# Kernel tuning notes

Measured on AMD Instinct MI355X. Metric: run time of the kernel, lower is better.

The kernel has to match this reference:

```python
import jax, jax.numpy as jnp
import numpy as np

B, C, H, W = 8, 256, 80, 160   # 1/8-resolution feature maps of a 640x1280 stereo pair
DISP = 192 // 8                 # cost volume depth at 1/8 res
FACTOR = 2 ** 3                 # convex-upsample factor (n_downsample=3)
TOP_K = 3


def setup_inputs() -> dict:
    key = jax.random.key(0)
    k1, k2, k3 = jax.random.split(key, 3)
    return {
        "left": jax.random.normal(k1, (B, C, H, W), dtype=jnp.float32),
        "right": jax.random.normal(k2, (B, C, H, W), dtype=jnp.float32),
        "mask": jax.random.normal(k3, (B, 9 * FACTOR * FACTOR, H, W), dtype=jnp.float32),
        "iters": 12,
    }


def build_cost_volume(left, right):
    # cost[b,i,h,w] = mean_c left[b,c,h,w] * right[b,c,h,w-i], zero where w < i
    slices = []
    for i in range(DISP):  # fixed small structural loop over disparity shifts
        prod = jnp.mean(left[:, :, :, i:] * right[:, :, :, : W - i if i > 0 else W], axis=1)
        prod = jnp.pad(prod, ((0, 0), (0, 0), (i, 0)))
        slices.append(prod)
    return jnp.stack(slices, axis=1)  # [B, DISP, H, W]


def regression_topk(cost, k=TOP_K):
    # top-k over the disparity axis, softmax-weighted expectation of indices
    c = jnp.moveaxis(cost, 1, -1)            # [B, H, W, DISP]
    vals, inds = jax.lax.top_k(c, k)          # descending, like torch sort(1, True)[:, :k]
    w = jax.nn.softmax(vals, axis=-1)
    disp = jnp.sum(w * inds.astype(vals.dtype), axis=-1)
    return disp[:, None]                      # [B, 1, H, W]


def convex_upsample(flow, mask, iters):
    # Upsample [H,W] flow -> [8H,8W] via softmax convex combination of 3x3 neighbors.
    N, D, Hh, Ww = flow.shape
    temp = 1.0 + jnp.exp(-(jnp.float32(iters) - 1.0))  # training-mode temperature
    m = mask.reshape(N, 1, 9, FACTOR, FACTOR, Hh, Ww)
    m = jax.nn.softmax(m / temp, axis=2)
    fp = jnp.pad(FACTOR * flow, ((0, 0), (0, 0), (1, 1), (1, 1)))
    # 3x3 unfold in torch F.unfold row-major order: (dy, dx)
    patches = jnp.stack(
        [fp[:, :, dy:dy + Hh, dx:dx + Ww] for dy in range(3) for dx in range(3)], axis=2
    )  # [N, D, 9, H, W]
    up = jnp.sum(m * patches[:, :, :, None, None], axis=2)   # [N, D, F, F, H, W]
    up = up.transpose(0, 1, 4, 2, 5, 3)                      # [N, D, H, F, W, F]
    return up.reshape(N, D, FACTOR * Hh, FACTOR * Ww)


def reference(left, right, mask, iters):
    cost = build_cost_volume(left, right)
    init_disp = regression_topk(cost)                               # [B,1,H,W]
    # flow field (x-disparity channel + frozen y channel, as delta_flow[:,1]=0)
    flow = jnp.concatenate([init_disp, jnp.zeros_like(init_disp)], axis=1)
    flow_up = convex_upsample(flow, mask, iters)                    # [B,2,8H,8W]
    return -flow_up[:, :1]                                          # disparity prediction
```

## Files before the change

### kernel.cpp

```cpp
#include <hip/hip_runtime.h>
#include <cmath>

#define NBATCH 8
#define NCH    256
#define NH     80
#define NW     160
#define NDISP  24
#define FAC    8

constexpr int TPB1  = 128;
constexpr int WPB   = 2;
constexpr int NTILE = 5;
constexpr int SLOTS = 192;
constexpr int NBUF  = 2;
constexpr int NSTEP = 16;

typedef __attribute__((address_space(1))) unsigned int gu32;
typedef __attribute__((address_space(3))) unsigned int lu32;

#define LDS_AUX 2

__device__ __forceinline__ void gload_lds16(const float* g, float4* l) {
  __builtin_amdgcn_global_load_lds((gu32*)g, (lu32*)l, 16, 0, LDS_AUX);
}

template <int N>
__device__ __forceinline__ void wait_vm() {
  if constexpr (N == 3)      asm volatile("s_waitcnt vmcnt(3)" ::: "memory");
  else                       asm volatile("s_waitcnt vmcnt(0)" ::: "memory");
  __builtin_amdgcn_sched_barrier(0);
}

__device__ __forceinline__ void wait_lgkm0() {
  asm volatile("s_waitcnt lgkmcnt(0)" ::: "memory");
  __builtin_amdgcn_sched_barrier(0);
}

__device__ __forceinline__ float f4c(const float4& v, int k) {
  switch (k) { case 0: return v.x; case 1: return v.y; case 2: return v.z; default: return v.w; }
}

__global__ __launch_bounds__(TPB1) void cost_topk_kernel(
    const float* __restrict__ left, const float* __restrict__ right,
    float* __restrict__ disp)
{
  __shared__ float4 lds4[WPB][NBUF][SLOTS];

  const int lane = threadIdx.x & 63;
  const int widx = threadIdx.x >> 6;
  const int tileid = blockIdx.x;
  const int tile = tileid % NTILE;
  const int row  = tileid / NTILE;
  const int b    = row / NH;
  const int h    = row % NH;
  const int wb   = tile * 32;
  const int chb  = widx * NSTEP;

  const int cg = lane & 7;
  const int wq = lane >> 3;

  const size_t hw = (size_t)NH * NW;
  const float* lrow = left  + (size_t)b * NCH * hw + (size_t)h * NW;
  const float* rrow = right + (size_t)b * NCH * hw + (size_t)h * NW;

  const int c0 = lane >> 4,        q0 = (lane & 15) ^ c0;
  const int c1 = 4 + (lane >> 4),  q1 = (lane & 15) ^ c1;
  const int cl = lane >> 3,        wqs = (lane & 7) ^ cl;

  int off0 = wb - 32 + 4 * q0; if (off0 < 0) off0 = 0;
  int off1 = wb - 32 + 4 * q1; if (off1 < 0) off1 = 0;

  const float* srcR0 = rrow + (size_t)(c0 * 32 + chb) * hw + off0;
  const float* srcR1 = rrow + (size_t)(c1 * 32 + chb) * hw + off1;
  const float* srcL  = lrow + (size_t)(cl * 32 + chb) * hw + wb + 4 * wqs;

  float4* const wbase = &lds4[widx][0][0];

#define STAGE(BP) do {                               \
    gload_lds16(srcR0, (BP));                        \
    gload_lds16(srcR1, (BP) + 64);                   \
    gload_lds16(srcL,  (BP) + 128);                  \
    srcR0 += hw; srcR1 += hw; srcL += hw; } while (0)

  int rsl[7];
#pragma unroll
  for (int k = 0; k < 7; ++k) rsl[k] = cg * 16 + ((wq + 2 + k) ^ cg);
  const int lslot = 128 + cg * 8 + (wq ^ cg);

  float acc[NDISP][4];
#pragma unroll
  for (int i = 0; i < NDISP; ++i)
#pragma unroll
    for (int ws = 0; ws < 4; ++ws) acc[i][ws] = 0.f;

  auto fmastep = [&](const float4* base) {
    float4 Lq = base[lslot];
    float4 Qa = base[rsl[0]];
#pragma unroll
    for (int g = 0; g < 6; ++g) {
      float4 Qb = base[rsl[g + 1]];
      const int i0 = 20 - 4 * g;
#pragma unroll
      for (int di = 0; di < 4; ++di)
#pragma unroll
        for (int ws = 0; ws < 4; ++ws) {
          const int pos = ws - di + 4;
          float rv = (pos < 4) ? f4c(Qa, pos) : f4c(Qb, pos - 4);
          acc[i0 + di][ws] = __builtin_fmaf(f4c(Lq, ws), rv, acc[i0 + di][ws]);
        }
      Qa = Qb;
    }
  };

  const float4 fzero{0.f, 0.f, 0.f, 0.f};
  const int azslot = (lane >> 3) * 16 + (lane & 7);

  STAGE(wbase + 0 * SLOTS);

#pragma unroll 2
  for (int j = 0; j < NSTEP; ++j) {
    wait_lgkm0();
    if (j + 1 < NSTEP) {
      STAGE(wbase + ((j + 1) & 1) * SLOTS);
      wait_vm<3>();
    } else {
      wait_vm<0>();
    }
    float4* bc = wbase + (j & 1) * SLOTS;
    if (tile == 0) bc[azslot] = fzero;
    fmastep(bc);
  }
#undef STAGE

#pragma unroll
  for (int mskm = 1; mskm < 8; mskm <<= 1)
#pragma unroll
    for (int i = 0; i < NDISP; ++i)
#pragma unroll
      for (int ws = 0; ws < 4; ++ws)
        acc[i][ws] += __shfl_xor(acc[i][ws], mskm, 64);

  if (widx == 1 && cg == 0) {
    float4* red = &lds4[1][0][0];
#pragma unroll
    for (int i = 0; i < NDISP; ++i)
      red[wq * NDISP + i] = float4{acc[i][0], acc[i][1], acc[i][2], acc[i][3]};
  }
  __syncthreads();

  if (widx == 0 && cg == 0) {
    const float4* red = &lds4[1][0][0];
    float o[4];
#pragma unroll
    for (int i = 0; i < NDISP; ++i) {
      float4 r = red[wq * NDISP + i];
      acc[i][0] += r.x; acc[i][1] += r.y; acc[i][2] += r.z; acc[i][3] += r.w;
    }
#pragma unroll
    for (int ws = 0; ws < 4; ++ws) {
      float v1 = -1e30f, v2 = -1e30f, v3 = -1e30f;
      int   j1 = 0, j2 = 0, j3 = 0;
#pragma unroll
      for (int i = 0; i < NDISP; ++i) {
        float v = acc[i][ws] * 0.00390625f;
        if (v > v1)      { v3 = v2; j3 = j2; v2 = v1; j2 = j1; v1 = v; j1 = i; }
        else if (v > v2) { v3 = v2; j3 = j2; v2 = v;  j2 = i; }
        else if (v > v3) { v3 = v;  j3 = i; }
      }
      float e2 = expf(v2 - v1), e3 = expf(v3 - v1);
      float ssum = 1.0f + e2 + e3;
      o[ws] = ((float)j1 + e2 * (float)j2 + e3 * (float)j3) / ssum;
    }
    *reinterpret_cast<float4*>(&disp[((size_t)b * NH + h) * NW + wb + wq * 4]) =
        float4{o[0], o[1], o[2], o[3]};
  }
}

__global__ __launch_bounds__(256) void upsample_kernel(
    const float* __restrict__ disp, const float* __restrict__ mask,
    const int* __restrict__ itp, float* __restrict__ out)
{
  int idx = blockIdx.x * 256 + threadIdx.x;
  const int w  = idx % NW;
  const int fy = (idx / NW) & 7;
  const int h  = (idx / (NW * FAC)) % NH;
  const int b  = idx / (NW * FAC * NH);

  const float iters = (float)itp[0];
  const float temp  = 1.0f + __expf(-(iters - 1.0f));
  const float sc    = 1.44269504088896340736f / temp;

  const size_t hw = (size_t)NH * NW;
  const float* drow = disp + (size_t)b * hw;
  float d[9];
#pragma unroll
  for (int dy = 0; dy < 3; ++dy)
#pragma unroll
    for (int dx = 0; dx < 3; ++dx) {
      int h2 = h + dy - 1, w2 = w + dx - 1;
      bool ok = (h2 >= 0) && (h2 < NH) && (w2 >= 0) && (w2 < NW);
      d[dy * 3 + dx] = ok ? drow[h2 * NW + w2] : 0.f;
    }

  const float* mb = mask + (size_t)b * 576 * hw + (size_t)h * NW + w;
  float m[9][FAC];
#pragma unroll
  for (int j = 0; j < 9; ++j)
#pragma unroll
    for (int fx = 0; fx < FAC; ++fx)
      m[j][fx] = mb[(size_t)((j * 8 + fy) * 8 + fx) * hw];

  float o[FAC];
#pragma unroll
  for (int fx = 0; fx < FAC; ++fx) {
    float mx = m[0][fx];
#pragma unroll
    for (int j = 1; j < 9; ++j) mx = fmaxf(mx, m[j][fx]);
    float ssum = 0.f, accv = 0.f;
#pragma unroll
    for (int j = 0; j < 9; ++j) {
      float e = exp2f((m[j][fx] - mx) * sc);
      ssum += e;
      accv += e * d[j];
    }
    o[fx] = (-8.0f * accv) * __builtin_amdgcn_rcpf(ssum);
  }

  float* op = out + ((size_t)b * (NH * FAC) + (size_t)(h * FAC + fy)) * (NW * FAC) + (size_t)w * FAC;
  *reinterpret_cast<float4*>(op)     = float4{o[0], o[1], o[2], o[3]};
  *reinterpret_cast<float4*>(op + 4) = float4{o[4], o[5], o[6], o[7]};
}

extern "C" void kernel_launch(void* const* d_in, const int* in_sizes, int n_in,
                              void* d_out, int out_size, void* d_ws, size_t ws_size,
                              hipStream_t stream) {
  (void)in_sizes; (void)n_in; (void)out_size; (void)ws_size;
  const float* left  = (const float*)d_in[0];
  const float* right = (const float*)d_in[1];
  const float* mask  = (const float*)d_in[2];
  const int*   iters = (const int*)d_in[3];
  float* out  = (float*)d_out;
  float* disp = (float*)d_ws;

  hipLaunchKernelGGL(cost_topk_kernel, dim3(NBATCH * NH * NTILE), dim3(TPB1), 0, stream,
                     left, right, disp);
  hipLaunchKernelGGL(upsample_kernel, dim3(NBATCH * NH * FAC * NW / 256), dim3(256), 0, stream,
                     disp, mask, iters, out);
}
```

Before: 130.2 us.

## Triple-buffer cost-volume LDS staging and use nontemporal mask loads and output stores

The cost kernel moves from double to triple buffering of the global-to-LDS loads, keeping two stages in flight with a vmcnt(6) wait and rotating buffer pointers. This is meant to hide more memory latency in the channel loop. The global_load_lds aux/cache-policy bits change from 2 to 0. The upsample kernel uses nontemporal loads for the streamed mask and nontemporal stores for the output to reduce cache pollution. Triple buffering raises LDS use per block, which may lower occupancy.

```diff
diff --git a/kernel.cpp b/kernel.cpp
--- a/kernel.cpp
+++ b/kernel.cpp
@@ -12,21 +12,21 @@
 constexpr int WPB   = 2;
 constexpr int NTILE = 5;
 constexpr int SLOTS = 192;
-constexpr int NBUF  = 2;
+constexpr int NBUF  = 3;
 constexpr int NSTEP = 16;
 
 typedef __attribute__((address_space(1))) unsigned int gu32;
 typedef __attribute__((address_space(3))) unsigned int lu32;
-
-#define LDS_AUX 2
+typedef float f4v __attribute__((ext_vector_type(4)));
 
 __device__ __forceinline__ void gload_lds16(const float* g, float4* l) {
-  __builtin_amdgcn_global_load_lds((gu32*)g, (lu32*)l, 16, 0, LDS_AUX);
+  __builtin_amdgcn_global_load_lds((gu32*)g, (lu32*)l, 16, 0, 0);
 }
 
 template <int N>
 __device__ __forceinline__ void wait_vm() {
-  if constexpr (N == 3)      asm volatile("s_waitcnt vmcnt(3)" ::: "memory");
+  if constexpr (N == 6)      asm volatile("s_waitcnt vmcnt(6)" ::: "memory");
+  else if constexpr (N == 3) asm volatile("s_waitcnt vmcnt(3)" ::: "memory");
   else                       asm volatile("s_waitcnt vmcnt(0)" ::: "memory");
   __builtin_amdgcn_sched_barrier(0);
 }
@@ -74,8 +74,6 @@
   const float* srcR1 = rrow + (size_t)(c1 * 32 + chb) * hw + off1;
   const float* srcL  = lrow + (size_t)(cl * 32 + chb) * hw + wb + 4 * wqs;
 
-  float4* const wbase = &lds4[widx][0][0];
-
 #define STAGE(BP) do {                               \
     gload_lds16(srcR0, (BP));                        \
     gload_lds16(srcR1, (BP) + 64);                   \
@@ -115,20 +113,32 @@
   const float4 fzero{0.f, 0.f, 0.f, 0.f};
   const int azslot = (lane >> 3) * 16 + (lane & 7);
 
-  STAGE(wbase + 0 * SLOTS);
-
-#pragma unroll 2
-  for (int j = 0; j < NSTEP; ++j) {
+  float4* bA = &lds4[widx][0][0];
+  float4* bB = &lds4[widx][1][0];
+  float4* bC = &lds4[widx][2][0];
+
+  STAGE(bA);
+  STAGE(bB);
+
+#pragma unroll 1
+  for (int j = 0; j < NSTEP - 2; ++j) {
     wait_lgkm0();
-    if (j + 1 < NSTEP) {
-      STAGE(wbase + ((j + 1) & 1) * SLOTS);
-      wait_vm<3>();
-    } else {
-      wait_vm<0>();
-    }
-    float4* bc = wbase + (j & 1) * SLOTS;
-    if (tile == 0) bc[azslot] = fzero;
-    fmastep(bc);
+    STAGE(bC);
+    wait_vm<6>();
+    if (tile == 0) bA[azslot] = fzero;
+    fmastep(bA);
+    float4* t = bA; bA = bB; bB = bC; bC = t;
+  }
+  {
+    wait_lgkm0(); wait_vm<3>();
+    if (tile == 0) bA[azslot] = fzero;
+    fmastep(bA);
+    float4* t = bA; bA = bB; bB = bC; bC = t;
+  }
+  {
+    wait_lgkm0(); wait_vm<0>();
+    if (tile == 0) bA[azslot] = fzero;
+    fmastep(bA);
   }
 #undef STAGE
 
@@ -208,7 +218,7 @@
   for (int j = 0; j < 9; ++j)
 #pragma unroll
     for (int fx = 0; fx < FAC; ++fx)
-      m[j][fx] = mb[(size_t)((j * 8 + fy) * 8 + fx) * hw];
+      m[j][fx] = __builtin_nontemporal_load(mb + (size_t)((j * 8 + fy) * 8 + fx) * hw);
 
   float o[FAC];
 #pragma unroll
@@ -227,8 +237,10 @@
   }
 
   float* op = out + ((size_t)b * (NH * FAC) + (size_t)(h * FAC + fy)) * (NW * FAC) + (size_t)w * FAC;
-  *reinterpret_cast<float4*>(op)     = float4{o[0], o[1], o[2], o[3]};
-  *reinterpret_cast<float4*>(op + 4) = float4{o[4], o[5], o[6], o[7]};
+  f4v v0 = {o[0], o[1], o[2], o[3]};
+  f4v v1 = {o[4], o[5], o[6], o[7]};
+  __builtin_nontemporal_store(v0, reinterpret_cast<f4v*>(op));
+  __builtin_nontemporal_store(v1, reinterpret_cast<f4v*>(op + 4));
 }
 
 extern "C" void kernel_launch(void* const* d_in, const int* in_sizes, int n_in,
```

Measured after the change: 127.7 us. No clear change (-1.9%).
